# Kernel optimization log

Measured on AMD Instinct MI355X. Metric: run time of the kernel, lower is better.

## Reference

```python
import jax, jax.numpy as jnp
import numpy as np

RHO = 100.0
W = 256
CHUNK = 64 * 64  # pixel tile size, as in the torch render loop


def _rot_matrices():
    # eulers ('zyx') used by the module; each has only one nonzero angle so
    # the scipy intrinsic/extrinsic distinction is moot.
    def Ry(t):
        c, s = np.cos(t), np.sin(t)
        return np.array([[c, 0, s], [0, 1, 0], [-s, 0, c]])

    def Rx(t):
        c, s = np.cos(t), np.sin(t)
        return np.array([[1, 0, 0], [0, c, -s], [0, s, c]])

    p = np.pi
    mats = [np.eye(3), Ry(p / 2), Ry(p), Ry(3 * p / 2), Rx(p / 2), Rx(3 * p / 2)]
    return np.stack(mats).astype(np.float32)  # [6,3,3]


def _pix_xy():
    idx = np.arange(W * W)
    i, j = idx // W, idx % W
    pix = np.stack([j, i], axis=1).astype(np.float32)  # [W2,2] (x=col, y=row)
    return (pix - W // 2 + 0.5) / (W // 2)


def _render(x, src_n, pix_chunks):
    # x: [N,3] rotated points; pix_chunks: [n_chunks, CHUNK, 2]
    depth = x[:, 2]
    dmin = jax.lax.stop_gradient(jnp.min(depth))  # torch uses .item() -> constant
    dmax = jax.lax.stop_gradient(jnp.max(depth))
    pix_val = 1.0 - (depth - dmin) / (dmax - dmin)  # [N]
    xy = x[:, :2]

    def chunk_fn(pxy):  # pxy: [CHUNK,2]
        d2 = jnp.sum((xy[:, None, :] - pxy[None, :, :]) ** 2, axis=-1)  # [N,CHUNK]
        wgt = jnp.exp(-d2 / 2 * RHO ** 2)
        v = pix_val[:, None] * wgt
        return jnp.max(v[:src_n], axis=0), jnp.max(v[src_n:], axis=0)

    src_img, tgt_img = jax.lax.map(jax.checkpoint(chunk_fn), pix_chunks)
    return jnp.stack([src_img.reshape(W, W), tgt_img.reshape(W, W)], axis=0)  # [2,W,W]


def setup_inputs() -> dict:
    key = jax.random.key(0)
    k1, k2 = jax.random.split(key)
    src_pred = jax.random.normal(k1, (4096, 3), dtype=jnp.float32)
    tgt_pcd = jax.random.normal(k2, (4096, 3), dtype=jnp.float32)
    return {"src_pred": src_pred, "tgt_pcd": tgt_pcd}


def reference(src_pred, tgt_pcd):
    rots = jnp.asarray(_rot_matrices())          # [6,3,3]
    pix_xy = jnp.asarray(_pix_xy())              # [W2,2]
    pix_chunks = pix_xy.reshape(-1, CHUNK, 2)    # [n_chunks, CHUNK, 2]
    registrated = jnp.concatenate([src_pred, tgt_pcd], axis=0)  # [N,3]
    src_n = src_pred.shape[0]
    imgs = []
    for v in range(rots.shape[0]):
        x = registrated @ rots[v].T  # == (rot @ pts.T).T
        img = _render(x, src_n, pix_chunks)
        imgs.append((img - 0.5) / 0.5)
    return jnp.stack(imgs, axis=0)  # [6,2,W,W]
```

## Files before the change

### kernel.cpp

```cpp
#include <hip/hip_runtime.h>
#include <math.h>


#define WIMG 256
#define HALF 4096
#define CLOG2 7213.475204444817f
#define INV_CLOG2 1.3862943611198906e-4f
#define RCUT 0.084f
#define SCAP 1024

static __device__ __constant__ float RMAT[6][9] = {
  { 1.f, 0.f, 0.f,   0.f, 1.f, 0.f,   0.f, 0.f, 1.f },
  { 6.123233995736766e-17f, 0.f, 1.f,  0.f, 1.f, 0.f,  -1.f, 0.f, 6.123233995736766e-17f },
  { -1.f, 0.f, 1.2246467991473532e-16f, 0.f, 1.f, 0.f, -1.2246467991473532e-16f, 0.f, -1.f },
  { -1.8369701987210297e-16f, 0.f, -1.f, 0.f, 1.f, 0.f,  1.f, 0.f, -1.8369701987210297e-16f },
  { 1.f, 0.f, 0.f,  0.f, 6.123233995736766e-17f, -1.f,  0.f, 1.f, 6.123233995736766e-17f },
  { 1.f, 0.f, 0.f,  0.f, -1.8369701987210297e-16f, 1.f, 0.f, -1.f, -1.8369701987210297e-16f },
};

__global__ __launch_bounds__(256) void fused_render(const float* __restrict__ src,
                                                    const float* __restrict__ tgt,
                                                    float* __restrict__ out) {
  __shared__ float4 sc[SCAP];
  __shared__ float smin[4], smax[4];
  __shared__ int s_n;

  const int b = blockIdx.x;
  const int vh = b >> 6;
  const int tile = (b + 21 * vh) & 63;
  const int v = vh >> 1, h = vh & 1;
  const int tx = tile & 3, ty = tile >> 2;
  const int col0 = tx << 6, row0 = ty << 4;
  const int tid = threadIdx.x;
  const int lane = tid & 63, w = tid >> 6;

  const float* R = RMAT[v];
  const float r00 = R[0], r01 = R[1], r02 = R[2];
  const float r10 = R[3], r11 = R[4], r12 = R[5];
  const float r20 = R[6], r21 = R[7], r22 = R[8];

  const float4* own4 = (const float4*)(h ? tgt : src);
  const float4* oth4 = (const float4*)(h ? src : tgt);

  float zmin = 3.0e38f, zmax = -3.0e38f;
  float4 q[12];
#pragma unroll
  for (int j = 0; j < 4; ++j) {
    const int t = tid + 256 * j;
    const float4 a = oth4[3 * t], bq = oth4[3 * t + 1], c = oth4[3 * t + 2];
    const float z0 = r20 * a.x  + r21 * a.y  + r22 * a.z;
    const float z1 = r20 * a.w  + r21 * bq.x + r22 * bq.y;
    const float z2 = r20 * bq.z + r21 * bq.w + r22 * c.x;
    const float z3 = r20 * c.y  + r21 * c.z  + r22 * c.w;
    zmin = fminf(zmin, fminf(fminf(z0, z1), fminf(z2, z3)));
    zmax = fmaxf(zmax, fmaxf(fmaxf(z0, z1), fmaxf(z2, z3)));
  }
#pragma unroll
  for (int j = 0; j < 4; ++j) {
    const int t = tid + 256 * j;
    q[3 * j]     = own4[3 * t];
    q[3 * j + 1] = own4[3 * t + 1];
    q[3 * j + 2] = own4[3 * t + 2];
    const float4 a = q[3 * j], bq = q[3 * j + 1], c = q[3 * j + 2];
    const float z0 = r20 * a.x  + r21 * a.y  + r22 * a.z;
    const float z1 = r20 * a.w  + r21 * bq.x + r22 * bq.y;
    const float z2 = r20 * bq.z + r21 * bq.w + r22 * c.x;
    const float z3 = r20 * c.y  + r21 * c.z  + r22 * c.w;
    zmin = fminf(zmin, fminf(fminf(z0, z1), fminf(z2, z3)));
    zmax = fmaxf(zmax, fmaxf(fmaxf(z0, z1), fmaxf(z2, z3)));
  }
#pragma unroll
  for (int off = 32; off > 0; off >>= 1) {
    zmin = fminf(zmin, __shfl_down(zmin, off));
    zmax = fmaxf(zmax, __shfl_down(zmax, off));
  }
  if (tid == 0) s_n = 0;
  if (lane == 0) { smin[w] = zmin; smax[w] = zmax; }
  __syncthreads();
  const float dmin = fminf(fminf(smin[0], smin[1]), fminf(smin[2], smin[3]));
  const float dmax = fmaxf(fmaxf(smax[0], smax[1]), fmaxf(smax[2], smax[3]));
  const float range = dmax - dmin;

  const float pxmin = (col0 - 127.5f) * 0.0078125f;
  const float pymin = (row0 - 127.5f) * 0.0078125f;
  const float bx0 = pxmin - RCUT, bx1 = pxmin + 63.0f * 0.0078125f + RCUT;
  const float by0 = pymin - RCUT, by1 = pymin + 15.0f * 0.0078125f + RCUT;
#pragma unroll
  for (int j = 0; j < 4; ++j) {
    const float4 a = q[3 * j], bq = q[3 * j + 1], c = q[3 * j + 2];
    float P[4][3] = { { a.x, a.y, a.z }, { a.w, bq.x, bq.y },
                      { bq.z, bq.w, c.x }, { c.y, c.z, c.w } };
#pragma unroll
    for (int e = 0; e < 4; ++e) {
      const float x = r00 * P[e][0] + r01 * P[e][1] + r02 * P[e][2];
      const float y = r10 * P[e][0] + r11 * P[e][1] + r12 * P[e][2];
      if (x >= bx0 && x <= bx1 && y >= by0 && y <= by1) {
        const float z = r20 * P[e][0] + r21 * P[e][1] + r22 * P[e][2];
        const float pv = 1.0f - (z - dmin) / range;
        const float pen = (pv > 0.f) ? (-log2f(pv) * INV_CLOG2) : 1.0e26f;
        const int idx = atomicAdd(&s_n, 1);
        if (idx < SCAP) sc[idx] = make_float4(x, y, pen, 0.f);
      }
    }
  }
  __syncthreads();
  const int total = min(s_n, SCAP);

  const float px  = (col0 + lane - 127.5f) * 0.0078125f;
  const float py0 = (row0 + w - 127.5f) * 0.0078125f;
  const float py1 = py0 + 0.03125f;
  const float py2 = py0 + 0.0625f;
  const float py3 = py0 + 0.09375f;
  float m0 = 3.0e38f, m1 = 3.0e38f, m2 = 3.0e38f, m3 = 3.0e38f;
  int k = 0;
  for (; k + 1 < total; k += 2) {
    const float4 A = sc[k];
    const float4 B = sc[k + 1];
    const float dxa = A.x - px; const float ca = fmaf(dxa, dxa, A.z);
    const float dxb = B.x - px; const float cb = fmaf(dxb, dxb, B.z);
    float da, db;
    da = A.y - py0; db = B.y - py0;
    m0 = fminf(fminf(m0, fmaf(da, da, ca)), fmaf(db, db, cb));
    da = A.y - py1; db = B.y - py1;
    m1 = fminf(fminf(m1, fmaf(da, da, ca)), fmaf(db, db, cb));
    da = A.y - py2; db = B.y - py2;
    m2 = fminf(fminf(m2, fmaf(da, da, ca)), fmaf(db, db, cb));
    da = A.y - py3; db = B.y - py3;
    m3 = fminf(fminf(m3, fmaf(da, da, ca)), fmaf(db, db, cb));
  }
  if (k < total) {
    const float4 A = sc[k];
    const float dxa = A.x - px; const float ca = fmaf(dxa, dxa, A.z);
    float da;
    da = A.y - py0; m0 = fminf(m0, fmaf(da, da, ca));
    da = A.y - py1; m1 = fminf(m1, fmaf(da, da, ca));
    da = A.y - py2; m2 = fminf(m2, fmaf(da, da, ca));
    da = A.y - py3; m3 = fminf(m3, fmaf(da, da, ca));
  }

  float* o = out + (vh * WIMG + row0 + w) * WIMG + col0 + lane;
  o[0]    = 2.0f * exp2f(-CLOG2 * m0) - 1.0f;
  o[1024] = 2.0f * exp2f(-CLOG2 * m1) - 1.0f;
  o[2048] = 2.0f * exp2f(-CLOG2 * m2) - 1.0f;
  o[3072] = 2.0f * exp2f(-CLOG2 * m3) - 1.0f;
}

extern "C" void kernel_launch(void* const* d_in, const int* in_sizes, int n_in,
                              void* d_out, int out_size, void* d_ws, size_t ws_size,
                              hipStream_t stream) {
  const float* src = (const float*)d_in[0];
  const float* tgt = (const float*)d_in[1];
  float* out = (float*)d_out;
  (void)d_ws; (void)ws_size;
  fused_render<<<768, 256, 0, stream>>>(src, tgt, out);
}
```

Baseline: 70.52 us.

## Switch from pixel-gather to point-scatter splatting with LDS atomicMin over row strips

Blocks now cover full-width 8-row strips (384 blocks instead of 768 tiles of 64x16). Instead of each pixel scanning every culled point, each candidate point scatters into only the pixels within the cutoff radius, using LDS atomicMin on the float bits of the exponent. The aim is to replace dense pixel-by-point distance work with sparse splatting. In exchange it adds LDS atomic contention and divergent inner loops, and the larger strip may overflow the 1024-entry candidate cap.

Measured after the change: 70.87 us. Within noise of the previous version (+0.5%).

```diff
diff --git a/kernel.cpp b/kernel.cpp
--- a/kernel.cpp
+++ b/kernel.cpp
@@ -7,7 +7,8 @@
 #define CLOG2 7213.475204444817f
 #define INV_CLOG2 1.3862943611198906e-4f
 #define RCUT 0.084f
-#define SCAP 1024
+#define QCAP 1024
+#define FBPAD 257
 
 static __device__ __constant__ float RMAT[6][9] = {
   { 1.f, 0.f, 0.f,   0.f, 1.f, 0.f,   0.f, 0.f, 1.f },
@@ -21,16 +22,16 @@
 __global__ __launch_bounds__(256) void fused_render(const float* __restrict__ src,
                                                     const float* __restrict__ tgt,
                                                     float* __restrict__ out) {
-  __shared__ float4 sc[SCAP];
+  __shared__ unsigned fbu[8 * FBPAD];
+  __shared__ float4 cq[QCAP];
   __shared__ float smin[4], smax[4];
   __shared__ int s_n;
 
   const int b = blockIdx.x;
-  const int vh = b >> 6;
-  const int tile = (b + 21 * vh) & 63;
+  const int vh = b >> 5;
+  const int strip = ((b & 31) + 13 * vh) & 31;
   const int v = vh >> 1, h = vh & 1;
-  const int tx = tile & 3, ty = tile >> 2;
-  const int col0 = tx << 6, row0 = ty << 4;
+  const int row0 = strip << 3;
   const int tid = threadIdx.x;
   const int lane = tid & 63, w = tid >> 6;
 
@@ -38,6 +39,9 @@
   const float r00 = R[0], r01 = R[1], r02 = R[2];
   const float r10 = R[3], r11 = R[4], r12 = R[5];
   const float r20 = R[6], r21 = R[7], r22 = R[8];
+
+  for (int i = tid; i < 8 * FBPAD; i += 256) fbu[i] = 0x7F800000u;
+  if (tid == 0) s_n = 0;
 
   const float4* own4 = (const float4*)(h ? tgt : src);
   const float4* oth4 = (const float4*)(h ? src : tgt);
@@ -74,75 +78,67 @@
     zmin = fminf(zmin, __shfl_down(zmin, off));
     zmax = fmaxf(zmax, __shfl_down(zmax, off));
   }
-  if (tid == 0) s_n = 0;
   if (lane == 0) { smin[w] = zmin; smax[w] = zmax; }
   __syncthreads();
   const float dmin = fminf(fminf(smin[0], smin[1]), fminf(smin[2], smin[3]));
   const float dmax = fmaxf(fmaxf(smax[0], smax[1]), fmaxf(smax[2], smax[3]));
   const float range = dmax - dmin;
 
-  const float pxmin = (col0 - 127.5f) * 0.0078125f;
-  const float pymin = (row0 - 127.5f) * 0.0078125f;
-  const float bx0 = pxmin - RCUT, bx1 = pxmin + 63.0f * 0.0078125f + RCUT;
-  const float by0 = pymin - RCUT, by1 = pymin + 15.0f * 0.0078125f + RCUT;
+  const float wy0 = (row0 - 127.5f) * 0.0078125f - RCUT;
+  const float wy1 = (row0 + 7 - 127.5f) * 0.0078125f + RCUT;
 #pragma unroll
   for (int j = 0; j < 4; ++j) {
     const float4 a = q[3 * j], bq = q[3 * j + 1], c = q[3 * j + 2];
-    float P[4][3] = { { a.x, a.y, a.z }, { a.w, bq.x, bq.y },
-                      { bq.z, bq.w, c.x }, { c.y, c.z, c.w } };
+    const float P[4][3] = { { a.x, a.y, a.z }, { a.w, bq.x, bq.y },
+                            { bq.z, bq.w, c.x }, { c.y, c.z, c.w } };
 #pragma unroll
     for (int e = 0; e < 4; ++e) {
       const float x = r00 * P[e][0] + r01 * P[e][1] + r02 * P[e][2];
       const float y = r10 * P[e][0] + r11 * P[e][1] + r12 * P[e][2];
-      if (x >= bx0 && x <= bx1 && y >= by0 && y <= by1) {
+      if (y >= wy0 && y <= wy1 && fabsf(x) <= 1.081f) {
         const float z = r20 * P[e][0] + r21 * P[e][1] + r22 * P[e][2];
         const float pv = 1.0f - (z - dmin) / range;
         const float pen = (pv > 0.f) ? (-log2f(pv) * INV_CLOG2) : 1.0e26f;
         const int idx = atomicAdd(&s_n, 1);
-        if (idx < SCAP) sc[idx] = make_float4(x, y, pen, 0.f);
+        if (idx < QCAP) cq[idx] = make_float4(x, y, pen, 0.f);
       }
     }
   }
   __syncthreads();
-  const int total = min(s_n, SCAP);
+  const int nc = min(s_n, QCAP);
 
-  const float px  = (col0 + lane - 127.5f) * 0.0078125f;
-  const float py0 = (row0 + w - 127.5f) * 0.0078125f;
-  const float py1 = py0 + 0.03125f;
-  const float py2 = py0 + 0.0625f;
-  const float py3 = py0 + 0.09375f;
-  float m0 = 3.0e38f, m1 = 3.0e38f, m2 = 3.0e38f, m3 = 3.0e38f;
-  int k = 0;
-  for (; k + 1 < total; k += 2) {
-    const float4 A = sc[k];
-    const float4 B = sc[k + 1];
-    const float dxa = A.x - px; const float ca = fmaf(dxa, dxa, A.z);
-    const float dxb = B.x - px; const float cb = fmaf(dxb, dxb, B.z);
-    float da, db;
-    da = A.y - py0; db = B.y - py0;
-    m0 = fminf(fminf(m0, fmaf(da, da, ca)), fmaf(db, db, cb));
-    da = A.y - py1; db = B.y - py1;
-    m1 = fminf(fminf(m1, fmaf(da, da, ca)), fmaf(db, db, cb));
-    da = A.y - py2; db = B.y - py2;
-    m2 = fminf(fminf(m2, fmaf(da, da, ca)), fmaf(db, db, cb));
-    da = A.y - py3; db = B.y - py3;
-    m3 = fminf(fminf(m3, fmaf(da, da, ca)), fmaf(db, db, cb));
+  const int r = tid >> 5;
+  const int ci = tid & 31;
+  const float py = (row0 + r - 127.5f) * 0.0078125f;
+  unsigned* fr = fbu + r * FBPAD;
+  for (int base = 0; base < nc; base += 32) {
+    const int k = base + ci;
+    if (k < nc) {
+      const float4 P = cq[k];
+      const float dy = P.y - py;
+      if (fabsf(dy) <= RCUT) {
+        const float dy2 = fmaf(dy, dy, P.z);
+        int c0 = (int)floorf(fmaf(P.x - RCUT, 128.0f, 127.5f));
+        int c1 = (int)ceilf (fmaf(P.x + RCUT, 128.0f, 127.5f));
+        c0 = max(c0, 0); c1 = min(c1, 255);
+        float px = fmaf((float)c0, 0.0078125f, -0.99609375f);
+        for (int c = c0; c <= c1; ++c) {
+          const float dx = P.x - px;
+          const float e = fmaf(dx, dx, dy2);
+          atomicMin(&fr[c], __float_as_uint(e));
+          px += 0.0078125f;
+        }
+      }
+    }
   }
-  if (k < total) {
-    const float4 A = sc[k];
-    const float dxa = A.x - px; const float ca = fmaf(dxa, dxa, A.z);
-    float da;
-    da = A.y - py0; m0 = fminf(m0, fmaf(da, da, ca));
-    da = A.y - py1; m1 = fminf(m1, fmaf(da, da, ca));
-    da = A.y - py2; m2 = fminf(m2, fmaf(da, da, ca));
-    da = A.y - py3; m3 = fminf(m3, fmaf(da, da, ca));
+  __syncthreads();
+
+  float* o = out + (vh * WIMG + row0) * WIMG;
+#pragma unroll
+  for (int i = 0; i < 8; ++i) {
+    const float e = __uint_as_float(fbu[i * FBPAD + tid]);
+    o[i * WIMG + tid] = 2.0f * exp2f(-CLOG2 * e) - 1.0f;
   }
-
-  float* o = out + (vh * WIMG + row0 + w) * WIMG + col0 + lane;
-  o[0]    = 2.0f * exp2f(-CLOG2 * m0) - 1.0f;
-  o[1024] = 2.0f * exp2f(-CLOG2 * m1) - 1.0f;
-  o[2048] = 2.0f * exp2f(-CLOG2 * m2) - 1.0f;
-  o[3072] = 2.0f * exp2f(-CLOG2 * m3) - 1.0f;
 }
 
 extern "C" void kernel_launch(void* const* d_in, const int* in_sizes, int n_in,
@@ -152,5 +148,5 @@
   const float* tgt = (const float*)d_in[1];
   float* out = (float*)d_out;
   (void)d_ws; (void)ws_size;
-  fused_render<<<768, 256, 0, stream>>>(src, tgt, out);
+  fused_render<<<384, 256, 0, stream>>>(src, tgt, out);
 }
```
